# Kernel optimization log

Hardware: AMD Instinct MI355X
Metric: run time of the kernel (lower is better)

Reference implementation:

```python
import jax, jax.numpy as jnp
import numpy as np

B, T, D, H = 2, 1024, 1024, 16
WINDOW = 32
KSZ = 2 * WINDOW + 1
MAXG = 32


def setup_inputs() -> dict:
    key = jax.random.key(0)
    ks = jax.random.split(key, 5)
    s = 0.02
    x = jax.random.normal(ks[0], (B, T, D), jnp.float32)
    Wq = jax.random.normal(ks[1], (D, D), jnp.float32) * s
    Wk = jax.random.normal(ks[2], (D, D), jnp.float32) * s
    Wv = jax.random.normal(ks[3], (D, D), jnp.float32) * s
    Wo = jax.random.normal(ks[4], (D, D), jnp.float32) * s
    # global tokens: one every T//MAXG positions (same for every batch row)
    global_mask = jnp.tile((jnp.arange(T) % (T // MAXG) == 0)[None, :], (B, 1))
    return {"x": x, "global_mask": global_mask, "Wq": Wq, "Wk": Wk,
            "Wv": Wv, "Wo": Wo, "maxG": MAXG}


def reference(x, global_mask, Wq, Wk, Wv, Wo, maxG):
    Bb, Tt, Dm = x.shape
    dh = Dm // H
    scale = dh ** -0.5

    def proj(W):
        return (x @ W.T).reshape(Bb, Tt, H, dh).transpose(0, 2, 1, 3)  # (B,H,T,dh)

    q, k, v = proj(Wq), proj(Wk), proj(Wv)

    # sliding windows via zero-padded gather (== F.unfold with padding=WINDOW)
    widx = jnp.arange(Tt)[:, None] + jnp.arange(KSZ)[None, :]  # index into padded axis

    def windows(t):
        tp = jnp.pad(t, ((0, 0), (0, 0), (WINDOW, WINDOW), (0, 0)))
        return tp[:, :, widx, :]  # (B,H,T,KSZ,dh)

    Kw, Vw = windows(k), windows(v)
    scores_local = jnp.einsum('bhtd,bhtwd->bhtw', q, Kw) * scale

    # pack global-token indices (stable argsort puts True positions first, in order)
    order = jnp.argsort(jnp.logical_not(global_mask), axis=1, stable=True)
    gidx = order[:, :maxG]                                   # (B,maxG)
    gvalid = jnp.take_along_axis(global_mask, gidx, axis=1)  # (B,maxG) bool
    gather_b = jax.vmap(lambda arr, i: arr[:, i, :])         # (H,T,dh),(maxG,)->(H,maxG,dh)
    Kg = gather_b(k, gidx) * gvalid[:, None, :, None]
    Vg = gather_b(v, gidx) * gvalid[:, None, :, None]

    scores_global = jnp.einsum('bhtd,bhgd->bhtg', q, Kg) * scale
    scores_global = jnp.where(gvalid[:, None, None, :], scores_global, -1e9)

    attn = jax.nn.softmax(jnp.concatenate([scores_local, scores_global], axis=-1), axis=-1)
    wl, wg = attn[..., :KSZ], attn[..., KSZ:]
    ctx = (jnp.einsum('bhtw,bhtwd->bhtd', wl, Vw)
           + jnp.einsum('bhtg,bhgd->bhtd', wg, Vg))
    out = ctx.transpose(0, 2, 1, 3).reshape(Bb, Tt, Dm) @ Wo.T

    # ---- debug full attention map (vectorized replica of the per-token loop) ----
    t = jnp.arange(Tt)
    left = jnp.maximum(0, t - WINDOW)
    win_len = jnp.minimum(Tt, t + WINDOW + 1) - left           # (T,)
    valid_w = jnp.arange(KSZ)[None, :] < win_len[:, None]      # (T,KSZ)
    s_loc = jnp.where(valid_w[None, None], scores_local, -jnp.inf)
    attn_d = jax.nn.softmax(jnp.concatenate([s_loc, scores_global], axis=-1), axis=-1)
    wl_d = attn_d[..., :KSZ] * valid_w[None, None]             # (B,H,T,KSZ)
    wg_d = attn_d[..., KSZ:] * gvalid[:, None, None, :]        # (B,H,T,maxG)
    cols = jnp.minimum(left[:, None] + jnp.arange(KSZ)[None, :], Tt - 1)  # (T,KSZ)
    rows = jnp.broadcast_to(t[:, None], (Tt, KSZ))
    full_attn = jnp.zeros((Bb, H, Tt, Tt), x.dtype)
    full_attn = full_attn.at[:, :, rows, cols].add(wl_d)
    full_attn = jax.vmap(lambda fa, w, gi: fa.at[:, :, gi].add(w))(full_attn, wg_d, gidx)
    return out, full_attn
```

## Files before the change

### kernel.cpp

```cpp
#include <hip/hip_runtime.h>

#define T_   1024
#define B_   2
#define H_   16
#define DH   64
#define D_   1024
#define WND  32
#define KSZ  65
#define NG   32

typedef float f32x4 __attribute__((ext_vector_type(4)));
typedef __bf16 bf16x8 __attribute__((ext_vector_type(8)));
typedef unsigned short u16x4 __attribute__((ext_vector_type(4)));

__device__ __forceinline__ unsigned short f2bf(float f) {
  unsigned u = __float_as_uint(f);
  return (unsigned short)((u + 0x7fffu + ((u >> 16) & 1u)) >> 16);
}

__global__ __launch_bounds__(256) void cvt_kernel(const float* __restrict__ x,
    const float* __restrict__ wq, const float* __restrict__ wk,
    const float* __restrict__ wv, const float* __restrict__ wo,
    unsigned short* __restrict__ dst) {
  int i4 = blockIdx.x * 256 + threadIdx.x;
  if (i4 >= (6 * 1048576) / 4) return;
  int idx = i4 * 4;
  int r = idx >> 20;
  const float* src; int off;
  if (r < 2)       { src = x;  off = idx; }
  else if (r == 2) { src = wq; off = idx - 2 * 1048576; }
  else if (r == 3) { src = wk; off = idx - 3 * 1048576; }
  else if (r == 4) { src = wv; off = idx - 4 * 1048576; }
  else             { src = wo; off = idx - 5 * 1048576; }
  f32x4 v = *(const f32x4*)(src + off);
  u16x4 o;
  o.x = f2bf(v[0]); o.y = f2bf(v[1]); o.z = f2bf(v[2]); o.w = f2bf(v[3]);
  *(u16x4*)(dst + idx) = o;
}

__global__ void gidx_kernel(const int* __restrict__ mask, int* __restrict__ gidx,
                            float* __restrict__ gval) {
  int b = blockIdx.x;
  int lane = threadIdx.x;
  const int* mb = mask + b * T_;
  unsigned long long lanemask = (1ull << lane) - 1ull;
  int base = 0;
  for (int c = 0; c < 16; ++c) {
    int t = c * 64 + lane;
    bool m = mb[t] != 0;
    unsigned long long bal = __ballot(m);
    int rank = __popcll(bal & lanemask);
    if (m && base + rank < NG) { gidx[b * NG + base + rank] = t; gval[b * NG + base + rank] = 1.f; }
    base += __popcll(bal);
    if (base >= NG) break;
  }
  int start = base < NG ? base : NG;
  if (start < NG) {
    base = start;
    for (int c = 0; c < 16; ++c) {
      int t = c * 64 + lane;
      bool m = mb[t] == 0;
      unsigned long long bal = __ballot(m);
      int rank = __popcll(bal & lanemask);
      if (m && base + rank < NG) { gidx[b * NG + base + rank] = t; gval[b * NG + base + rank] = 0.f; }
      base += __popcll(bal);
      if (base >= NG) break;
    }
  }
}

template<int MODE, int BM>
__global__ __launch_bounds__(256) void gemm128(const unsigned short* __restrict__ A,
    const unsigned short* __restrict__ B0, const unsigned short* __restrict__ B1,
    const unsigned short* __restrict__ B2,
    void* __restrict__ C0v, void* __restrict__ C1v, void* __restrict__ C2v) {
  constexpr int K = 1024;
  constexpr int FM = BM / 32;
  constexpr int ACH = BM * 8 / 256;
  constexpr int WM = BM / 2;
  __shared__ __attribute__((aligned(16))) unsigned short As[BM * 64];
  __shared__ __attribute__((aligned(16))) unsigned short Bs[128 * 64];

  int m0 = blockIdx.x * BM, n0 = blockIdx.y * 128;
  int zz = (MODE == 0) ? blockIdx.z : 0;
  const unsigned short* Bm;
  if (MODE == 0) Bm = (zz == 0) ? B0 : ((zz == 1) ? B1 : B2);
  else Bm = B0;

  int tid = threadIdx.x;
  int w = tid >> 6, l = tid & 63;
  int wr = w >> 1, wc = w & 1;
  int lr = l & 15, kg = l >> 4;

  f32x4 acc[FM][4] = {};

  for (int kt = 0; kt < K; kt += 64) {
    __syncthreads();
#pragma unroll
    for (int i = 0; i < ACH; ++i) {
      int ci = tid + 256 * i;
      int row = ci >> 3, c8 = ci & 7;
      *(bf16x8*)&As[row * 64 + ((c8 ^ (row & 7)) * 8)] =
          *(const bf16x8*)&A[(size_t)(m0 + row) * K + kt + c8 * 8];
    }
#pragma unroll
    for (int i = 0; i < 4; ++i) {
      int ci = tid + 256 * i;
      int row = ci >> 3, c8 = ci & 7;
      *(bf16x8*)&Bs[row * 64 + ((c8 ^ (row & 7)) * 8)] =
          *(const bf16x8*)&Bm[(size_t)(n0 + row) * K + kt + c8 * 8];
    }
    __syncthreads();
#pragma unroll
    for (int kk = 0; kk < 2; ++kk) {
      int c8 = kk * 4 + kg;
      bf16x8 af[FM], bfr[4];
#pragma unroll
      for (int mi = 0; mi < FM; ++mi) {
        int row = wr * WM + mi * 16 + lr;
        af[mi] = *(bf16x8*)&As[row * 64 + ((c8 ^ (row & 7)) * 8)];
      }
#pragma unroll
      for (int ni = 0; ni < 4; ++ni) {
        int row = wc * 64 + ni * 16 + lr;
        bfr[ni] = *(bf16x8*)&Bs[row * 64 + ((c8 ^ (row & 7)) * 8)];
      }
#pragma unroll
      for (int mi = 0; mi < FM; ++mi)
#pragma unroll
        for (int ni = 0; ni < 4; ++ni)
          acc[mi][ni] = __builtin_amdgcn_mfma_f32_16x16x32_bf16(af[mi], bfr[ni], acc[mi][ni], 0, 0, 0);
    }
  }

#pragma unroll
  for (int mi = 0; mi < FM; ++mi) {
#pragma unroll
    for (int ni = 0; ni < 4; ++ni) {
      int mbase = m0 + wr * WM + mi * 16 + (l >> 4) * 4;
      int n = n0 + wc * 64 + ni * 16 + (l & 15);
      if (MODE == 0) {
        unsigned short* C = (unsigned short*)((zz == 0) ? C0v : ((zz == 1) ? C1v : C2v));
        int b = mbase >> 10, t = mbase & 1023, h = n >> 6, d = n & 63;
        if (zz < 2) {
#pragma unroll
          for (int r = 0; r < 4; ++r)
            C[(((size_t)(b * H_ + h) * T_) + t + r) * DH + d] = f2bf(acc[mi][ni][r]);
        } else {
          u16x4 st;
          st.x = f2bf(acc[mi][ni][0]); st.y = f2bf(acc[mi][ni][1]);
          st.z = f2bf(acc[mi][ni][2]); st.w = f2bf(acc[mi][ni][3]);
          *(u16x4*)&C[(((size_t)(b * H_ + h) * DH) + d) * T_ + t] = st;
        }
      } else {
        float* C = (float*)C0v;
#pragma unroll
        for (int r = 0; r < 4; ++r)
          C[(size_t)(mbase + r) * 1024 + n] = acc[mi][ni][r];
      }
    }
  }
}

__global__ __launch_bounds__(512, 4) void attn_kernel(
    const unsigned short* __restrict__ qg, const unsigned short* __restrict__ kg_,
    const unsigned short* __restrict__ vg,
    const int* __restrict__ gidx_g, const float* __restrict__ gval_g,
    unsigned short* __restrict__ ctxb, float* __restrict__ fa) {
  int tid = threadIdx.x;
  int t0 = blockIdx.x * 32;
  int h = blockIdx.y, b = blockIdx.z;
  int lane = tid & 63, wv = tid >> 6;

  __shared__ __attribute__((aligned(16))) unsigned short QbL[32 * 64];
  __shared__ __attribute__((aligned(16))) unsigned short KbL[128 * 64];
  __shared__ __attribute__((aligned(16))) unsigned short VtL[64 * 128];
  __shared__ __attribute__((aligned(16))) unsigned short WbL[32 * 128];
  __shared__ __attribute__((aligned(16))) float Sf[32][132];
  __shared__ float m_out_s[32], invdo_s[32], rowfac_s[32];
  __shared__ int   gidx_s[32];
  __shared__ float gval_s[32];

  if (tid < 32) { gidx_s[tid] = gidx_g[b * NG + tid]; gval_s[tid] = gval_g[b * NG + tid]; }
  ((unsigned long long*)WbL)[tid] = 0ull;
  ((unsigned long long*)WbL)[tid + 512] = 0ull;
  __syncthreads();

  const unsigned short* qbh = qg + (size_t)(b * H_ + h) * T_ * DH;
  const unsigned short* kbh = kg_ + (size_t)(b * H_ + h) * T_ * DH;
  const unsigned short* vbh = vg + (size_t)(b * H_ + h) * DH * T_;

  if (tid < 256) {
    int r = tid >> 3, c8 = tid & 7;
    bf16x8 v = *(const bf16x8*)(qbh + (t0 + r) * 64 + c8 * 8);
    *(bf16x8*)((char*)QbL + ((r * 128 + c8 * 16) ^ ((r & 7) << 4))) = v;
  }
#pragma unroll
  for (int it = 0; it < 2; ++it) {
    int fi = tid + it * 512;
    int r = fi >> 3, c8 = fi & 7;
    int col; bool valid;
    if (r < 96) { col = t0 - 32 + r; valid = (col >= 0 && col < T_); }
    else { int g = r - 96; valid = gval_s[g] > 0.f; col = valid ? gidx_s[g] : 0; }
    bf16x8 v = {};
    if (valid) v = *(const bf16x8*)(kbh + col * 64 + c8 * 8);
    *(bf16x8*)((char*)KbL + ((r * 128 + c8 * 16) ^ ((r & 7) << 4))) = v;
  }
#pragma unroll
  for (int it = 0; it < 2; ++it) {
    int fi = tid + it * 512;
    if (fi < 768) {
      int d = fi / 12, rc = fi % 12;
      int cb = t0 - 32 + rc * 8;
      bf16x8 v = {};
      if (cb >= 0 && cb < T_) v = *(const bf16x8*)(vbh + d * T_ + cb);
      *(bf16x8*)((char*)VtL + ((d * 256 + rc * 16) ^ ((d & 7) << 4))) = v;
    }
  }
#pragma unroll
  for (int it = 0; it < 4; ++it) {
    int fi = tid + it * 512;
    int d = fi >> 5, g = fi & 31;
    unsigned short v = 0;
    if (gval_s[g] > 0.f) v = vbh[d * T_ + gidx_s[g]];
    *(unsigned short*)((char*)VtL + ((d * 256 + (96 + g) * 2) ^ ((d & 7) << 4))) = v;
  }
  __syncthreads();

  {
    int mt = wv & 1, nq = wv >> 1;
    int lr = lane & 15, kgl = lane >> 4;
    int arow = mt * 16 + lr;
    f32x4 acc0 = {}, acc1 = {};
#pragma unroll
    for (int s = 0; s < 2; ++s) {
      int c = s * 4 + kgl;
      bf16x8 a = *(bf16x8*)((char*)QbL + ((arow * 128 + c * 16) ^ ((arow & 7) << 4)));
      int br0 = nq * 32 + lr, br1 = nq * 32 + 16 + lr;
      bf16x8 b0 = *(bf16x8*)((char*)KbL + ((br0 * 128 + c * 16) ^ ((br0 & 7) << 4)));
      bf16x8 b1 = *(bf16x8*)((char*)KbL + ((br1 * 128 + c * 16) ^ ((br1 & 7) << 4)));
      acc0 = __builtin_amdgcn_mfma_f32_16x16x32_bf16(a, b0, acc0, 0, 0, 0);
      acc1 = __builtin_amdgcn_mfma_f32_16x16x32_bf16(a, b1, acc1, 0, 0, 0);
    }
    int orow = mt * 16 + (lane >> 4) * 4;
#pragma unroll
    for (int i = 0; i < 4; ++i) {
      Sf[orow + i][nq * 32 + lr] = acc0[i] * 0.125f;
      Sf[orow + i][nq * 32 + 16 + lr] = acc1[i] * 0.125f;
    }
  }
  __syncthreads();

  {
    int r = tid >> 4, lg = tid & 15;
    int t_abs = t0 + r;
    int left = (t_abs - WND > 0) ? (t_abs - WND) : 0;
    int tmp = t_abs + WND + 1; if (tmp > T_) tmp = T_;
    int wl = tmp - left;
    float sv[8]; bool vld[8], vdd[8];
#pragma unroll
    for (int ii = 0; ii < 8; ++ii) {
      int c = lg + ii * 16;
      bool loc = (c >= r && c <= r + 64);
      bool glob = (c >= 96);
      float s = Sf[r][c];
      if (glob && !(gval_s[c - 96] > 0.f)) s = -1e9f;
      vld[ii] = loc || glob;
      vdd[ii] = loc ? ((c - r) < wl) : glob;
      sv[ii] = s;
    }
    float mo = -1e30f, md = -1e30f;
#pragma unroll
    for (int ii = 0; ii < 8; ++ii) {
      if (vld[ii]) mo = fmaxf(mo, sv[ii]);
      if (vdd[ii]) md = fmaxf(md, sv[ii]);
    }
#pragma unroll
    for (int o = 1; o < 16; o <<= 1) {
      mo = fmaxf(mo, __shfl_xor(mo, o, 16));
      md = fmaxf(md, __shfl_xor(md, o, 16));
    }
    float eo = 0.f, ed = 0.f;
#pragma unroll
    for (int ii = 0; ii < 8; ++ii) {
      if (vld[ii]) eo += __expf(sv[ii] - mo);
      if (vdd[ii]) ed += __expf(sv[ii] - md);
    }
#pragma unroll
    for (int o = 1; o < 16; o <<= 1) {
      eo += __shfl_xor(eo, o, 16);
      ed += __shfl_xor(ed, o, 16);
    }
    if (lg == 0) {
      m_out_s[r] = mo;
      invdo_s[r] = 1.f / eo;
      rowfac_s[r] = (eo / ed) * __expf(mo - md);
    }
  }
  __syncthreads();

  for (int idx = tid; idx < 32 * 97; idx += 512) {
    int t = idx / 97;
    int j = idx - t * 97;
    int cc = (j < KSZ) ? (t + j) : (j + 31);
    float s = Sf[t][cc];
    float wgt = __expf(s - m_out_s[t]) * invdo_s[t];
    Sf[t][cc] = wgt;
    *(unsigned short*)((char*)WbL + ((t * 256 + cc * 2) ^ ((t & 7) << 4))) = f2bf(wgt);
  }
  __syncthreads();

  {
    int mt = wv >> 1, nt = wv & 1;
    int lr = lane & 15, kgl = lane >> 4;
    int arow = mt * 16 + lr;
    int brow = nt * 16 + lr;
    f32x4 acc = {};
#pragma unroll
    for (int s = 0; s < 4; ++s) {
      int c = s * 4 + kgl;
      bf16x8 a = *(bf16x8*)((char*)VtL + ((arow * 256 + c * 16) ^ ((arow & 7) << 4)));
      bf16x8 bb = *(bf16x8*)((char*)WbL + ((brow * 256 + c * 16) ^ ((brow & 7) << 4)));
      acc = __builtin_amdgcn_mfma_f32_16x16x32_bf16(a, bb, acc, 0, 0, 0);
    }
    int t = nt * 16 + lr;
    int dbase = mt * 16 + (lane >> 4) * 4;
    u16x4 st;
    st.x = f2bf(acc[0]); st.y = f2bf(acc[1]); st.z = f2bf(acc[2]); st.w = f2bf(acc[3]);
    *(u16x4*)(ctxb + ((size_t)(b * T_ + t0 + t)) * D_ + h * DH + dbase) = st;
  }

  {
    int rp = tid >> 8;
    int c0 = (tid & 255) * 4;
    unsigned gm = 0;
#pragma unroll
    for (int g = 0; g < NG; ++g) {
      int gc = gidx_s[g];
      if (gval_s[g] > 0.f && gc >= c0 && gc < c0 + 4) gm |= (1u << g);
    }
#pragma unroll 2
    for (int rr = 0; rr < 16; ++rr) {
      int r = rr * 2 + rp;
      int t_abs = t0 + r;
      int left = (t_abs - WND > 0) ? (t_abs - WND) : 0;
      int tmp = t_abs + WND + 1; if (tmp > T_) tmp = T_;
      int wl = tmp - left;
      float rf = rowfac_s[r];
      f32x4 o = {0.f, 0.f, 0.f, 0.f};
      int jj0 = c0 - left;
      if (jj0 > -4 && jj0 < wl) {
#pragma unroll
        for (int e = 0; e < 4; ++e) {
          int jj = jj0 + e;
          if (jj >= 0 && jj < wl) o[e] = Sf[r][r + jj] * rf;
        }
      }
      if (gm) {
        unsigned mm = gm;
        while (mm) {
          int g = __ffs(mm) - 1; mm &= mm - 1;
          int e = gidx_s[g] - c0;
          o[e] += Sf[r][96 + g] * rf;
        }
      }
      float* dst = fa + (((size_t)(b * H_ + h) * T_) + t_abs) * T_ + c0;
      *(f32x4*)dst = o;
    }
  }
}

extern "C" void kernel_launch(void* const* d_in, const int* in_sizes, int n_in,
                              void* d_out, int out_size, void* d_ws, size_t ws_size,
                              hipStream_t stream) {
  const float* x   = (const float*)d_in[0];
  const int* gmask = (const int*)d_in[1];
  const float* wq  = (const float*)d_in[2];
  const float* wk  = (const float*)d_in[3];
  const float* wv  = (const float*)d_in[4];
  const float* wo  = (const float*)d_in[5];

  char* ws = (char*)d_ws;
  unsigned short* bfarena = (unsigned short*)ws;
  unsigned short* xb  = bfarena;
  unsigned short* wqb = bfarena + 2 * 1048576;
  unsigned short* wkb = bfarena + 3 * 1048576;
  unsigned short* wvb = bfarena + 4 * 1048576;
  unsigned short* wob = bfarena + 5 * 1048576;
  unsigned short* qb  = bfarena + 6 * 1048576;
  unsigned short* kb  = qb + 2 * 1048576;
  unsigned short* vtb = kb + 2 * 1048576;
  unsigned short* ctxb = vtb + 2 * 1048576;
  int*   gidx = (int*)(ctxb + 2 * 1048576);
  float* gval = (float*)(gidx + 64);

  float* outp = (float*)d_out;
  float* fa   = outp + 2097152;

  cvt_kernel<<<dim3(6144), dim3(256), 0, stream>>>(x, wq, wk, wv, wo, bfarena);
  gidx_kernel<<<dim3(2), dim3(64), 0, stream>>>(gmask, gidx, gval);
  gemm128<0, 128><<<dim3(16, 8, 3), dim3(256), 0, stream>>>(xb, wqb, wkb, wvb, qb, kb, vtb);
  attn_kernel<<<dim3(32, 16, 2), dim3(512), 0, stream>>>(qb, kb, vtb, gidx, gval, ctxb, fa);
  gemm128<1, 64><<<dim3(32, 8, 1), dim3(256), 0, stream>>>(ctxb, wob, wob, wob, outp, outp, outp);
}
```

Before: 96.16 us.

## Fuse fp32-to-bf16 conversion and global-index build into projection GEMMs

Removes the separate conversion kernel and global-index kernel. The GEMMs now load fp32 x and weights and convert to bf16 while staging into shared memory, and the global-index pass runs in an extra grid column of the QKV GEMM. Q and K are stored row-major (B,T,D), so their epilogue and the attention loads use strided rows. V's transposed write goes through a shared-memory transpose so it can use vectorized stores. This saves two launches and one round trip of the bf16 copies, but doubles global read bytes per GEMM tile and recomputes the weight conversion in every tile.

New measurement: 95.02 us. About the same (-1.2%).

```diff
diff --git a/kernel.cpp b/kernel.cpp
--- a/kernel.cpp
+++ b/kernel.cpp
@@ -11,6 +11,7 @@
 
 typedef float f32x4 __attribute__((ext_vector_type(4)));
 typedef __bf16 bf16x8 __attribute__((ext_vector_type(8)));
+typedef __bf16 bf16x4 __attribute__((ext_vector_type(4)));
 typedef unsigned short u16x4 __attribute__((ext_vector_type(4)));
 
 __device__ __forceinline__ unsigned short f2bf(float f) {
@@ -18,74 +19,68 @@
   return (unsigned short)((u + 0x7fffu + ((u >> 16) & 1u)) >> 16);
 }
 
-__global__ __launch_bounds__(256) void cvt_kernel(const float* __restrict__ x,
-    const float* __restrict__ wq, const float* __restrict__ wk,
-    const float* __restrict__ wv, const float* __restrict__ wo,
-    unsigned short* __restrict__ dst) {
-  int i4 = blockIdx.x * 256 + threadIdx.x;
-  if (i4 >= (6 * 1048576) / 4) return;
-  int idx = i4 * 4;
-  int r = idx >> 20;
-  const float* src; int off;
-  if (r < 2)       { src = x;  off = idx; }
-  else if (r == 2) { src = wq; off = idx - 2 * 1048576; }
-  else if (r == 3) { src = wk; off = idx - 3 * 1048576; }
-  else if (r == 4) { src = wv; off = idx - 4 * 1048576; }
-  else             { src = wo; off = idx - 5 * 1048576; }
-  f32x4 v = *(const f32x4*)(src + off);
-  u16x4 o;
-  o.x = f2bf(v[0]); o.y = f2bf(v[1]); o.z = f2bf(v[2]); o.w = f2bf(v[3]);
-  *(u16x4*)(dst + idx) = o;
+template<bool F32>
+__device__ __forceinline__ bf16x8 load_cvt8(const char* p) {
+  if constexpr (F32) {
+    f32x4 a = *(const f32x4*)p;
+    f32x4 b = *(const f32x4*)(p + 16);
+    bf16x8 r;
+    r[0] = (__bf16)a[0]; r[1] = (__bf16)a[1]; r[2] = (__bf16)a[2]; r[3] = (__bf16)a[3];
+    r[4] = (__bf16)b[0]; r[5] = (__bf16)b[1]; r[6] = (__bf16)b[2]; r[7] = (__bf16)b[3];
+    return r;
+  } else {
+    return *(const bf16x8*)p;
+  }
 }
 
-__global__ void gidx_kernel(const int* __restrict__ mask, int* __restrict__ gidx,
-                            float* __restrict__ gval) {
-  int b = blockIdx.x;
-  int lane = threadIdx.x;
-  const int* mb = mask + b * T_;
-  unsigned long long lanemask = (1ull << lane) - 1ull;
-  int base = 0;
-  for (int c = 0; c < 16; ++c) {
-    int t = c * 64 + lane;
-    bool m = mb[t] != 0;
-    unsigned long long bal = __ballot(m);
-    int rank = __popcll(bal & lanemask);
-    if (m && base + rank < NG) { gidx[b * NG + base + rank] = t; gval[b * NG + base + rank] = 1.f; }
-    base += __popcll(bal);
-    if (base >= NG) break;
-  }
-  int start = base < NG ? base : NG;
-  if (start < NG) {
-    base = start;
-    for (int c = 0; c < 16; ++c) {
-      int t = c * 64 + lane;
-      bool m = mb[t] == 0;
-      unsigned long long bal = __ballot(m);
-      int rank = __popcll(bal & lanemask);
-      if (m && base + rank < NG) { gidx[b * NG + base + rank] = t; gval[b * NG + base + rank] = 0.f; }
-      base += __popcll(bal);
-      if (base >= NG) break;
-    }
-  }
-}
-
-template<int MODE, int BM>
-__global__ __launch_bounds__(256) void gemm128(const unsigned short* __restrict__ A,
-    const unsigned short* __restrict__ B0, const unsigned short* __restrict__ B1,
-    const unsigned short* __restrict__ B2,
-    void* __restrict__ C0v, void* __restrict__ C1v, void* __restrict__ C2v) {
+template<int MODE, int BM, bool AF32, bool BF32>
+__global__ __launch_bounds__(256) void gemm128(
+    const void* __restrict__ A,
+    const void* __restrict__ B0, const void* __restrict__ B1, const void* __restrict__ B2,
+    void* __restrict__ C0v, void* __restrict__ C1v, void* __restrict__ C2v,
+    const int* __restrict__ mask, int* __restrict__ gidxo, float* __restrict__ gvalo) {
   constexpr int K = 1024;
   constexpr int FM = BM / 32;
   constexpr int ACH = BM * 8 / 256;
   constexpr int WM = BM / 2;
-  __shared__ __attribute__((aligned(16))) unsigned short As[BM * 64];
-  __shared__ __attribute__((aligned(16))) unsigned short Bs[128 * 64];
+  constexpr int AE = AF32 ? 4 : 2, BE = BF32 ? 4 : 2;
+
+  if (MODE == 0 && blockIdx.x == 16) {
+    if (blockIdx.y == 0 && blockIdx.z == 0 && threadIdx.x < 128) {
+      int b = threadIdx.x >> 6, lane = threadIdx.x & 63;
+      const int* mb = mask + b * T_;
+      unsigned long long lanemask = (1ull << lane) - 1ull;
+      int base = 0;
+      for (int c = 0; c < 16 && base < NG; ++c) {
+        int t = c * 64 + lane;
+        bool m = mb[t] != 0;
+        unsigned long long bal = __ballot(m);
+        int rank = __popcll(bal & lanemask);
+        if (m && base + rank < NG) { gidxo[b*NG+base+rank] = t; gvalo[b*NG+base+rank] = 1.f; }
+        base += __popcll(bal);
+      }
+      if (base < NG) {
+        for (int c = 0; c < 16 && base < NG; ++c) {
+          int t = c * 64 + lane;
+          bool m = mb[t] == 0;
+          unsigned long long bal = __ballot(m);
+          int rank = __popcll(bal & lanemask);
+          if (m && base + rank < NG) { gidxo[b*NG+base+rank] = t; gvalo[b*NG+base+rank] = 0.f; }
+          base += __popcll(bal);
+        }
+      }
+    }
+    return;
+  }
+
+  __shared__ __attribute__((aligned(16))) unsigned short SMEM[BM * 64 + 128 * 64];
+  unsigned short* As = SMEM;
+  unsigned short* Bs = SMEM + BM * 64;
 
   int m0 = blockIdx.x * BM, n0 = blockIdx.y * 128;
   int zz = (MODE == 0) ? blockIdx.z : 0;
-  const unsigned short* Bm;
-  if (MODE == 0) Bm = (zz == 0) ? B0 : ((zz == 1) ? B1 : B2);
-  else Bm = B0;
+  const char* Ab = (const char*)A;
+  const char* Bb = (const char*)((MODE == 0) ? (zz == 0 ? B0 : (zz == 1 ? B1 : B2)) : B0);
 
   int tid = threadIdx.x;
   int w = tid >> 6, l = tid & 63;
@@ -101,14 +96,14 @@
       int ci = tid + 256 * i;
       int row = ci >> 3, c8 = ci & 7;
       *(bf16x8*)&As[row * 64 + ((c8 ^ (row & 7)) * 8)] =
-          *(const bf16x8*)&A[(size_t)(m0 + row) * K + kt + c8 * 8];
+          load_cvt8<AF32>(Ab + ((size_t)(m0 + row) * K + kt + c8 * 8) * AE);
     }
 #pragma unroll
     for (int i = 0; i < 4; ++i) {
       int ci = tid + 256 * i;
       int row = ci >> 3, c8 = ci & 7;
       *(bf16x8*)&Bs[row * 64 + ((c8 ^ (row & 7)) * 8)] =
-          *(const bf16x8*)&Bm[(size_t)(n0 + row) * K + kt + c8 * 8];
+          load_cvt8<BF32>(Bb + ((size_t)(n0 + row) * K + kt + c8 * 8) * BE);
     }
     __syncthreads();
 #pragma unroll
@@ -133,31 +128,56 @@
     }
   }
 
-#pragma unroll
-  for (int mi = 0; mi < FM; ++mi) {
-#pragma unroll
-    for (int ni = 0; ni < 4; ++ni) {
-      int mbase = m0 + wr * WM + mi * 16 + (l >> 4) * 4;
-      int n = n0 + wc * 64 + ni * 16 + (l & 15);
-      if (MODE == 0) {
-        unsigned short* C = (unsigned short*)((zz == 0) ? C0v : ((zz == 1) ? C1v : C2v));
-        int b = mbase >> 10, t = mbase & 1023, h = n >> 6, d = n & 63;
-        if (zz < 2) {
-#pragma unroll
-          for (int r = 0; r < 4; ++r)
-            C[(((size_t)(b * H_ + h) * T_) + t + r) * DH + d] = f2bf(acc[mi][ni][r]);
-        } else {
-          u16x4 st;
-          st.x = f2bf(acc[mi][ni][0]); st.y = f2bf(acc[mi][ni][1]);
-          st.z = f2bf(acc[mi][ni][2]); st.w = f2bf(acc[mi][ni][3]);
-          *(u16x4*)&C[(((size_t)(b * H_ + h) * DH) + d) * T_ + t] = st;
-        }
-      } else {
-        float* C = (float*)C0v;
+  if (MODE == 1) {
+    float* C = (float*)C0v;
+#pragma unroll
+    for (int mi = 0; mi < FM; ++mi)
+#pragma unroll
+      for (int ni = 0; ni < 4; ++ni) {
+        int mbase = m0 + wr * WM + mi * 16 + (l >> 4) * 4;
+        int n = n0 + wc * 64 + ni * 16 + lr;
 #pragma unroll
         for (int r = 0; r < 4; ++r)
           C[(size_t)(mbase + r) * 1024 + n] = acc[mi][ni][r];
       }
+  } else if (zz < 2) {
+    unsigned short* C = (unsigned short*)(zz == 0 ? C0v : C1v);
+#pragma unroll
+    for (int mi = 0; mi < FM; ++mi)
+#pragma unroll
+      for (int ni = 0; ni < 4; ++ni) {
+        int mbase = m0 + wr * WM + mi * 16 + (l >> 4) * 4;
+        int n = n0 + wc * 64 + ni * 16 + lr;
+#pragma unroll
+        for (int r = 0; r < 4; ++r) {
+          __bf16 v = (__bf16)acc[mi][ni][r];
+          C[(size_t)(mbase + r) * 1024 + n] = *(unsigned short*)&v;
+        }
+      }
+  } else {
+    __syncthreads();
+    char* Tb = (char*)SMEM;
+#pragma unroll
+    for (int mi = 0; mi < FM; ++mi)
+#pragma unroll
+      for (int ni = 0; ni < 4; ++ni) {
+        int mb2 = wr * WM + mi * 16 + (l >> 4) * 4;
+        int nl = wc * 64 + ni * 16 + lr;
+        bf16x4 pk;
+        pk[0] = (__bf16)acc[mi][ni][0]; pk[1] = (__bf16)acc[mi][ni][1];
+        pk[2] = (__bf16)acc[mi][ni][2]; pk[3] = (__bf16)acc[mi][ni][3];
+        *(bf16x4*)(Tb + ((nl * 256 + mb2 * 2) ^ ((nl & 7) << 4))) = pk;
+      }
+    __syncthreads();
+    unsigned short* C = (unsigned short*)C2v;
+    int bb = m0 >> 10, tbase = m0 & 1023;
+#pragma unroll
+    for (int it = 0; it < 8; ++it) {
+      int ci = tid + 256 * it;
+      int dl = ci >> 4, tc = ci & 15;
+      bf16x8 v = *(bf16x8*)(Tb + ((dl * 256 + tc * 16) ^ ((dl & 7) << 4)));
+      int n = n0 + dl, hh = n >> 6, dd = n & 63;
+      *(bf16x8*)&C[((size_t)(bb * H_ + hh) * DH + dd) * T_ + tbase + tc * 8] = v;
     }
   }
 }
@@ -186,13 +206,13 @@
   ((unsigned long long*)WbL)[tid + 512] = 0ull;
   __syncthreads();
 
-  const unsigned short* qbh = qg + (size_t)(b * H_ + h) * T_ * DH;
-  const unsigned short* kbh = kg_ + (size_t)(b * H_ + h) * T_ * DH;
+  const unsigned short* qbh = qg + (size_t)(b * T_ + t0) * D_ + h * DH;
+  const unsigned short* kbh = kg_ + (size_t)(b * T_) * D_ + h * DH;
   const unsigned short* vbh = vg + (size_t)(b * H_ + h) * DH * T_;
 
   if (tid < 256) {
     int r = tid >> 3, c8 = tid & 7;
-    bf16x8 v = *(const bf16x8*)(qbh + (t0 + r) * 64 + c8 * 8);
+    bf16x8 v = *(const bf16x8*)(qbh + (size_t)r * D_ + c8 * 8);
     *(bf16x8*)((char*)QbL + ((r * 128 + c8 * 16) ^ ((r & 7) << 4))) = v;
   }
 #pragma unroll
@@ -203,7 +223,7 @@
     if (r < 96) { col = t0 - 32 + r; valid = (col >= 0 && col < T_); }
     else { int g = r - 96; valid = gval_s[g] > 0.f; col = valid ? gidx_s[g] : 0; }
     bf16x8 v = {};
-    if (valid) v = *(const bf16x8*)(kbh + col * 64 + c8 * 8);
+    if (valid) v = *(const bf16x8*)(kbh + (size_t)col * D_ + c8 * 8);
     *(bf16x8*)((char*)KbL + ((r * 128 + c8 * 16) ^ ((r & 7) << 4))) = v;
   }
 #pragma unroll
@@ -229,14 +249,14 @@
 
   {
     int mt = wv & 1, nq = wv >> 1;
-    int lr = lane & 15, kgl = lane >> 4;
-    int arow = mt * 16 + lr;
+    int lrr = lane & 15, kgl = lane >> 4;
+    int arow = mt * 16 + lrr;
     f32x4 acc0 = {}, acc1 = {};
 #pragma unroll
     for (int s = 0; s < 2; ++s) {
       int c = s * 4 + kgl;
       bf16x8 a = *(bf16x8*)((char*)QbL + ((arow * 128 + c * 16) ^ ((arow & 7) << 4)));
-      int br0 = nq * 32 + lr, br1 = nq * 32 + 16 + lr;
+      int br0 = nq * 32 + lrr, br1 = nq * 32 + 16 + lrr;
       bf16x8 b0 = *(bf16x8*)((char*)KbL + ((br0 * 128 + c * 16) ^ ((br0 & 7) << 4)));
       bf16x8 b1 = *(bf16x8*)((char*)KbL + ((br1 * 128 + c * 16) ^ ((br1 & 7) << 4)));
       acc0 = __builtin_amdgcn_mfma_f32_16x16x32_bf16(a, b0, acc0, 0, 0, 0);
@@ -245,8 +265,8 @@
     int orow = mt * 16 + (lane >> 4) * 4;
 #pragma unroll
     for (int i = 0; i < 4; ++i) {
-      Sf[orow + i][nq * 32 + lr] = acc0[i] * 0.125f;
-      Sf[orow + i][nq * 32 + 16 + lr] = acc1[i] * 0.125f;
+      Sf[orow + i][nq * 32 + lrr] = acc0[i] * 0.125f;
+      Sf[orow + i][nq * 32 + 16 + lrr] = acc1[i] * 0.125f;
     }
   }
   __syncthreads();
@@ -312,9 +332,9 @@
 
   {
     int mt = wv >> 1, nt = wv & 1;
-    int lr = lane & 15, kgl = lane >> 4;
-    int arow = mt * 16 + lr;
-    int brow = nt * 16 + lr;
+    int lrr = lane & 15, kgl = lane >> 4;
+    int arow = mt * 16 + lrr;
+    int brow = nt * 16 + lrr;
     f32x4 acc = {};
 #pragma unroll
     for (int s = 0; s < 4; ++s) {
@@ -323,7 +343,7 @@
       bf16x8 bb = *(bf16x8*)((char*)WbL + ((brow * 256 + c * 16) ^ ((brow & 7) << 4)));
       acc = __builtin_amdgcn_mfma_f32_16x16x32_bf16(a, bb, acc, 0, 0, 0);
     }
-    int t = nt * 16 + lr;
+    int t = nt * 16 + lrr;
     int dbase = mt * 16 + (lane >> 4) * 4;
     u16x4 st;
     st.x = f2bf(acc[0]); st.y = f2bf(acc[1]); st.z = f2bf(acc[2]); st.w = f2bf(acc[3]);
@@ -381,15 +401,9 @@
   const float* wo  = (const float*)d_in[5];
 
   char* ws = (char*)d_ws;
-  unsigned short* bfarena = (unsigned short*)ws;
-  unsigned short* xb  = bfarena;
-  unsigned short* wqb = bfarena + 2 * 1048576;
-  unsigned short* wkb = bfarena + 3 * 1048576;
-  unsigned short* wvb = bfarena + 4 * 1048576;
-  unsigned short* wob = bfarena + 5 * 1048576;
-  unsigned short* qb  = bfarena + 6 * 1048576;
-  unsigned short* kb  = qb + 2 * 1048576;
-  unsigned short* vtb = kb + 2 * 1048576;
+  unsigned short* qb   = (unsigned short*)ws;
+  unsigned short* kb   = qb + 2 * 1048576;
+  unsigned short* vtb  = kb + 2 * 1048576;
   unsigned short* ctxb = vtb + 2 * 1048576;
   int*   gidx = (int*)(ctxb + 2 * 1048576);
   float* gval = (float*)(gidx + 64);
@@ -397,9 +411,9 @@
   float* outp = (float*)d_out;
   float* fa   = outp + 2097152;
 
-  cvt_kernel<<<dim3(6144), dim3(256), 0, stream>>>(x, wq, wk, wv, wo, bfarena);
-  gidx_kernel<<<dim3(2), dim3(64), 0, stream>>>(gmask, gidx, gval);
-  gemm128<0, 128><<<dim3(16, 8, 3), dim3(256), 0, stream>>>(xb, wqb, wkb, wvb, qb, kb, vtb);
+  gemm128<0, 128, true, true><<<dim3(17, 8, 3), dim3(256), 0, stream>>>(
+      x, wq, wk, wv, qb, kb, vtb, gmask, gidx, gval);
   attn_kernel<<<dim3(32, 16, 2), dim3(512), 0, stream>>>(qb, kb, vtb, gidx, gval, ctxb, fa);
-  gemm128<1, 64><<<dim3(32, 8, 1), dim3(256), 0, stream>>>(ctxb, wob, wob, wob, outp, outp, outp);
+  gemm128<1, 64, false, true><<<dim3(32, 8, 1), dim3(256), 0, stream>>>(
+      ctxb, wo, wo, wo, outp, outp, outp, nullptr, nullptr, nullptr);
 }
```
